# Performance work log

Measured on AMD Instinct MI355X. Metric: run time of the kernel, lower is better.

## Reference

```python
import jax, jax.numpy as jnp
import numpy as np
from jax import lax

E = 192      # hidden size
NH = 6       # attention heads
L = 6        # mixer blocks (permutation length)
CO = 256     # merging output channels
KH, KW = 7, 11   # locality window
LOCAL = (False, False, True, True, True, True)
B, H, W = 64, 8, 64


def skew(x, pad_value):
    # shift every row one step right, turning columns into diagonals (torch skew)
    rest = x.shape[:-2]
    Hd, Wd = x.shape[-2], x.shape[-1]
    x = jnp.pad(x, [(0, 0)] * (x.ndim - 1) + [(0, Hd)], constant_values=pad_value)
    x = x.reshape(*rest, -1)[..., : Hd * (Hd + Wd - 1)]
    x = x.reshape(*rest, Hd, Hd + Wd - 1)
    end = (Hd + Wd - 1) - (Wd // 2) + (Wd % 2 - 1)
    return x[..., Wd // 2 : end]


def make_mask(h, w, kh, kw):
    # boolean [h*w, h*w]; True inside the local window (torch: True = NOT allowed)
    m = jnp.ones((h, w, kh, kw), dtype=bool)
    m = m.transpose(0, 2, 1, 3)        # [h, kh, w, kw]
    m = skew(m, 0)                     # [h, kh, w, w]
    m = m.transpose(2, 3, 0, 1)        # [w, w, h, kh]
    m = skew(m, 0)                     # [w, w, h, h]
    m = m.transpose(2, 0, 3, 1)        # [h, w, h, w]
    return m.reshape(h * w, h * w)


def layernorm(x, g, b, eps=1e-5):
    mu = jnp.mean(x, axis=-1, keepdims=True)
    var = jnp.mean((x - mu) ** 2, axis=-1, keepdims=True)
    return (x - mu) / jnp.sqrt(var + eps) * g + b


def mha(x, mask, wi, bi, wo, bo, nh):
    # torch nn.MultiheadAttention (batch_first, self-attn, inference)
    b, s, e = x.shape
    hd = e // nh
    qkv = x @ wi.T + bi                                   # [b, s, 3e]
    q, k, v = jnp.split(qkv, 3, axis=-1)
    to_heads = lambda t: t.reshape(b, s, nh, hd).transpose(0, 2, 1, 3)
    q, k, v = to_heads(q), to_heads(k), to_heads(v)
    scores = jnp.einsum('bhqd,bhkd->bhqk', q, k) / jnp.sqrt(jnp.asarray(hd, x.dtype))
    if mask is not None:
        scores = jnp.where(mask, -jnp.inf, scores)
    attn = jax.nn.softmax(scores, axis=-1)
    out = jnp.einsum('bhqk,bhkd->bhqd', attn, v)
    out = out.transpose(0, 2, 1, 3).reshape(b, s, e)
    return out @ wo.T + bo


def mixer_block(x, mask, wi, bi, wo, bo, g1, b1, g2, b2, wm1, bm1, wm2, bm2):
    x = layernorm(x, g1, b1)
    x = mha(x, mask, wi, bi, wo, bo, NH) + x
    x = layernorm(x, g2, b2)
    h = jax.nn.relu(x @ wm1.T + bm1)
    return h @ wm2.T + bm2 + x


def fvtr_stage(image, in_w, in_b, out_w, out_b, ln1_g, ln1_b, ln2_g, ln2_b,
               w1, b1, w2, b2, conv_w, conv_b, mln_g, mln_b):
    bsz, c, h, w = image.shape
    x = jnp.swapaxes(image, -1, -3).reshape(bsz, w * h, c)   # [B, W*H, C]
    mask = make_mask(h, w, KH, KW)
    for i, loc in enumerate(LOCAL):
        x = mixer_block(x, mask if loc else None,
                        in_w[i], in_b[i], out_w[i], out_b[i],
                        ln1_g[i], ln1_b[i], ln2_g[i], ln2_b[i],
                        w1[i], b1[i], w2[i], b2[i])
    x = jnp.swapaxes(x.reshape(bsz, w, h, c), -1, -3)        # [B, C, H, W]
    # MergingBlock: conv (3,1) stride (2,1) pad (1,0) + channel LayerNorm
    y = lax.conv_general_dilated(x, conv_w, window_strides=(2, 1),
                                 padding=((1, 1), (0, 0)),
                                 dimension_numbers=('NCHW', 'OIHW', 'NCHW'))
    y = y + conv_b[None, :, None, None]
    y = jnp.moveaxis(y, 1, -1)
    y = layernorm(y, mln_g, mln_b)
    return jnp.moveaxis(y, -1, 1)


def setup_inputs() -> dict:
    key = jax.random.key(0)
    ks = jax.random.split(key, 8)
    s = 0.02
    return {
        'image': jax.random.normal(ks[0], (B, E, H, W), jnp.float32),
        'in_w':  s * jax.random.normal(ks[1], (L, 3 * E, E), jnp.float32),
        'in_b':  jnp.zeros((L, 3 * E), jnp.float32),
        'out_w': s * jax.random.normal(ks[2], (L, E, E), jnp.float32),
        'out_b': jnp.zeros((L, E), jnp.float32),
        'ln1_g': jnp.ones((L, E), jnp.float32),
        'ln1_b': jnp.zeros((L, E), jnp.float32),
        'ln2_g': jnp.ones((L, E), jnp.float32),
        'ln2_b': jnp.zeros((L, E), jnp.float32),
        'w1':    s * jax.random.normal(ks[3], (L, 4 * E, E), jnp.float32),
        'b1':    jnp.zeros((L, 4 * E), jnp.float32),
        'w2':    s * jax.random.normal(ks[4], (L, E, 4 * E), jnp.float32),
        'b2':    jnp.zeros((L, E), jnp.float32),
        'conv_w': s * jax.random.normal(ks[5], (CO, E, 3, 1), jnp.float32),
        'conv_b': jnp.zeros((CO,), jnp.float32),
        'mln_g': jnp.ones((CO,), jnp.float32),
        'mln_b': jnp.zeros((CO,), jnp.float32),
    }


def reference(image, in_w, in_b, out_w, out_b, ln1_g, ln1_b, ln2_g, ln2_b,
              w1, b1, w2, b2, conv_w, conv_b, mln_g, mln_b):
    return fvtr_stage(image, in_w, in_b, out_w, out_b, ln1_g, ln1_b, ln2_g, ln2_b,
                      w1, b1, w2, b2, conv_w, conv_b, mln_g, mln_b)
```

## Files before the change

### kernel.cpp

```cpp
#include <hip/hip_runtime.h>
#include <hip/hip_bf16.h>
#include <math.h>

#define Bn   64
#define Ssz  512
#define Ed   192
#define NHd  6
#define HDd  32
#define Ld   6
#define COd  256
#define Himg 8
#define Wimg 64
#define Mrows (Bn*Ssz)

typedef unsigned int  uint;
typedef unsigned short ushort;
using short8 = __attribute__((ext_vector_type(8))) short;
using f32x4  = __attribute__((ext_vector_type(4))) float;

__device__ inline ushort f2b(float f) {
    uint u = __builtin_bit_cast(uint, f);
    u = (u + 0x7FFFu + ((u >> 16) & 1u)) >> 16;
    return (ushort)u;
}

__device__ __forceinline__ float fexp2(float x) {
#if __has_builtin(__builtin_amdgcn_exp2f)
    return __builtin_amdgcn_exp2f(x);
#else
    return exp2f(x);
#endif
}

__device__ __forceinline__ uint cvt_pk_bf16(float a, float b) {
    uint r;
    asm("v_cvt_pk_bf16_f32 %0, %1, %2" : "=v"(r) : "v"(a), "v"(b));
    return r;
}

__device__ __forceinline__ void gload16(const ushort* g, ushort* l, int lane) {
#if __has_builtin(__builtin_amdgcn_global_load_lds)
    __builtin_amdgcn_global_load_lds(
        (const __attribute__((address_space(1))) uint*)g,
        (__attribute__((address_space(3))) uint*)l, 16, 0, 0);
#else
    *(uint4*)(l + (size_t)lane * 8) = *(const uint4*)g;
#endif
}

__global__ __launch_bounds__(256) void reshape_in(const float* __restrict__ img,
                                                  float* __restrict__ X) {
    int t = blockIdx.x * 256 + threadIdx.x;
    int c = t % Ed;
    int s = (t / Ed) % Ssz;
    int b = t / (Ed * Ssz);
    int w = s >> 3, h = s & 7;
    X[t] = img[(((size_t)b * Ed + c) * Himg + h) * Wimg + w];
}

__global__ __launch_bounds__(256) void f2b_arr(const float* __restrict__ in,
                                               ushort* __restrict__ out, int n) {
    int t = blockIdx.x * 256 + threadIdx.x;
    if (t < n) out[t] = f2b(in[t]);
}

__global__ __launch_bounds__(256) void conv_w_to_bf16(const float* __restrict__ cw,
                                                      ushort* __restrict__ out) {
    int t = blockIdx.x * 256 + threadIdx.x;
    if (t >= COd * 576) return;
    int co = t / 576, rem = t % 576;
    int kh = rem / Ed, c = rem % Ed;
    out[t] = f2b(cw[((size_t)co * Ed + c) * 3 + kh]);
}

__global__ __launch_bounds__(256) void ln_kernel(const float* __restrict__ in,
                                                 float* __restrict__ out,
                                                 ushort* __restrict__ outb,
                                                 const float* __restrict__ g,
                                                 const float* __restrict__ bb) {
    int row  = blockIdx.x * 4 + (threadIdx.x >> 6);
    int lane = threadIdx.x & 63;
    bool act = lane < 48;
    float4 v = make_float4(0.f, 0.f, 0.f, 0.f);
    if (act) v = ((const float4*)(in + (size_t)row * Ed))[lane];
    float s = v.x + v.y + v.z + v.w;
    #pragma unroll
    for (int off = 32; off > 0; off >>= 1) s += __shfl_xor(s, off);
    float mu = s * (1.f / 192.f);
    float4 d = make_float4(v.x - mu, v.y - mu, v.z - mu, v.w - mu);
    float qv = act ? (d.x*d.x + d.y*d.y + d.z*d.z + d.w*d.w) : 0.f;
    #pragma unroll
    for (int off = 32; off > 0; off >>= 1) qv += __shfl_xor(qv, off);
    float rstd = rsqrtf(qv * (1.f / 192.f) + 1e-5f);
    if (act) {
        float4 gg  = ((const float4*)g)[lane];
        float4 bbv = ((const float4*)bb)[lane];
        float4 y = make_float4(d.x * rstd * gg.x + bbv.x,
                               d.y * rstd * gg.y + bbv.y,
                               d.z * rstd * gg.z + bbv.z,
                               d.w * rstd * gg.w + bbv.w);
        ((float4*)(out + (size_t)row * Ed))[lane] = y;
        ushort4 yb;
        yb.x = f2b(y.x); yb.y = f2b(y.y); yb.z = f2b(y.z); yb.w = f2b(y.w);
        *(ushort4*)(outb + (size_t)row * Ed + lane * 4) = yb;
    }
}

template<int RELU, int RESID, int OBF, int VOUT>
__global__ __launch_bounds__(256) void gemm_mfma(
    const ushort* __restrict__ A, const ushort* __restrict__ Wt,
    const float* __restrict__ bias, const float* __restrict__ resid,
    float* __restrict__ C, ushort* __restrict__ Cb,
    ushort* __restrict__ qpout, ushort* __restrict__ kpout,
    ushort* __restrict__ vtout,
    int M, int N, int K)
{
    __shared__ __align__(16) ushort As[12288];
    __shared__ __align__(16) ushort Bs[6144];
    const int tid  = threadIdx.x;
    const int lane = tid & 63;
    const int wave = tid >> 6;
    const int wr = wave >> 1, wc = wave & 1;
    const int bm = blockIdx.x * 128;
    const int bn = blockIdx.y * 64;

    const ushort* Ag[6]; ushort* Al[6];
    #pragma unroll
    for (int i = 0; i < 6; ++i) {
        int fa = 4 * i + wave;
        int msub = fa / 3, ksub = fa % 3;
        int m = msub * 16 + (lane & 15);
        int k = ksub * 32 + ((lane >> 4) << 3);
        Ag[i] = A + (size_t)(bm + m) * K + k;
        Al[i] = As + fa * 512;
    }
    const ushort* Bg[3]; ushort* Bl[3];
    #pragma unroll
    for (int i = 0; i < 3; ++i) {
        int fb = 4 * i + wave;
        int nsub = fb / 3, ksub = fb % 3;
        int n = nsub * 16 + (lane & 15);
        int k = ksub * 32 + ((lane >> 4) << 3);
        Bg[i] = Wt + (size_t)(bn + n) * K + k;
        Bl[i] = Bs + fb * 512;
    }

    f32x4 acc[4][2];
    #pragma unroll
    for (int i = 0; i < 4; ++i)
        #pragma unroll
        for (int j = 0; j < 2; ++j) acc[i][j] = (f32x4){0.f, 0.f, 0.f, 0.f};

    for (int k0 = 0; k0 < K; k0 += 96) {
        #pragma unroll
        for (int i = 0; i < 6; ++i) gload16(Ag[i] + k0, Al[i], lane);
        #pragma unroll
        for (int i = 0; i < 3; ++i) gload16(Bg[i] + k0, Bl[i], lane);
        __syncthreads();
        #pragma unroll
        for (int ksub = 0; ksub < 3; ++ksub) {
            short8 af[4], bf[2];
            #pragma unroll
            for (int ms = 0; ms < 4; ++ms)
                af[ms] = *(const short8*)(As + (((wr*4+ms)*3 + ksub) * 64 + lane) * 8);
            #pragma unroll
            for (int ns = 0; ns < 2; ++ns)
                bf[ns] = *(const short8*)(Bs + (((wc*2+ns)*3 + ksub) * 64 + lane) * 8);
            #pragma unroll
            for (int ms = 0; ms < 4; ++ms)
                #pragma unroll
                for (int ns = 0; ns < 2; ++ns)
                    acc[ms][ns] = __builtin_amdgcn_mfma_f32_16x16x32_bf16(
                        af[ms], bf[ns], acc[ms][ns], 0, 0, 0);
        }
        __syncthreads();
    }

    int q = lane >> 4, colL = lane & 15;
    #pragma unroll
    for (int ms = 0; ms < 4; ++ms) {
        #pragma unroll
        for (int ns = 0; ns < 2; ++ns) {
            int row0 = bm + (wr*4 + ms) * 16 + q * 4;
            int col  = bn + (wc*2 + ns) * 16 + colL;
            float bvv = bias[col];
            float v[4];
            #pragma unroll
            for (int r = 0; r < 4; ++r) {
                v[r] = acc[ms][ns][r] + bvv;
                if (RELU) v[r] = fmaxf(v[r], 0.f);
                if (RESID) v[r] += resid[(size_t)(row0 + r) * N + col];
            }
            if (VOUT) {
                int bidx = row0 >> 9, srow = row0 & 511;
                if (col >= 384) {
                    int hh = (col - 384) >> 5, dd = (col - 384) & 31;
                    ushort4 pv;
                    pv.x = f2b(v[0]); pv.y = f2b(v[1]); pv.z = f2b(v[2]); pv.w = f2b(v[3]);
                    *(ushort4*)(vtout + (((size_t)(bidx * NHd + hh) * 32 + dd) << 9) + srow) = pv;
                } else {
                    ushort* dst = (col < 192) ? qpout : kpout;
                    int cc = (col < 192) ? col : col - 192;
                    if (col < 192) {
                        const float c2 = 0.2550547270628364f;
                        #pragma unroll
                        for (int r = 0; r < 4; ++r) v[r] *= c2;
                    }
                    int hh = cc >> 5, dd = cc & 31;
                    ushort* p = dst + ((size_t)(bidx * NHd + hh) << 14) + (size_t)srow * 32 + dd;
                    p[0]  = f2b(v[0]); p[32] = f2b(v[1]);
                    p[64] = f2b(v[2]); p[96] = f2b(v[3]);
                }
            } else {
                #pragma unroll
                for (int r = 0; r < 4; ++r) {
                    if (OBF) Cb[(size_t)(row0 + r) * N + col] = f2b(v[r]);
                    else     C [(size_t)(row0 + r) * N + col] = v[r];
                }
            }
        }
    }
}

template<int KIT, int LNOUT>
__global__ __launch_bounds__(256) void gemm_ln(
    const ushort* __restrict__ A, const ushort* __restrict__ Wt,
    const float* __restrict__ bias, const float* __restrict__ resid,
    const float* __restrict__ lng, const float* __restrict__ lnb,
    float* __restrict__ outf, ushort* __restrict__ outb)
{
    __shared__ __align__(16) ushort As[4096];
    __shared__ __align__(16) ushort Bs[12288];
    const int K = KIT * 64;
    const int lane = threadIdx.x & 63;
    const int wave = threadIdx.x >> 6;
    const int g = lane >> 4, ql = lane & 15;
    const int bm = blockIdx.x * 64;

    const ushort* Gp[8]; ushort* Lp[8];
    #pragma unroll
    for (int i = 0; i < 8; ++i) {
        int f = 4 * i + wave;
        if (f < 8) {
            int msub = f >> 1, ksub = f & 1;
            Gp[i] = A + (size_t)(bm + msub * 16 + ql) * K + ksub * 32 + g * 8;
            Lp[i] = As + f * 512;
        } else {
            int fb = f - 8, nsub = fb >> 1, ksub = fb & 1;
            Gp[i] = Wt + (size_t)(nsub * 16 + ql) * K + ksub * 32 + g * 8;
            Lp[i] = Bs + fb * 512;
        }
    }

    f32x4 acc[12];
    #pragma unroll
    for (int i = 0; i < 12; ++i) acc[i] = (f32x4){0.f, 0.f, 0.f, 0.f};

    for (int kc = 0; kc < KIT; ++kc) {
        #pragma unroll
        for (int i = 0; i < 8; ++i) gload16(Gp[i] + kc * 64, Lp[i], lane);
        __syncthreads();
        #pragma unroll
        for (int ksub = 0; ksub < 2; ++ksub) {
            short8 af = *(const short8*)(As + ((wave * 2 + ksub) * 64 + lane) * 8);
            #pragma unroll
            for (int ns = 0; ns < 12; ++ns) {
                short8 bf = *(const short8*)(Bs + ((ns * 2 + ksub) * 64 + lane) * 8);
                acc[ns] = __builtin_amdgcn_mfma_f32_16x16x32_bf16(af, bf, acc[ns], 0, 0, 0);
            }
        }
        __syncthreads();
    }

    float bi[12], gg[12], bb[12];
    #pragma unroll
    for (int ns = 0; ns < 12; ++ns) {
        int col = ns * 16 + ql;
        bi[ns] = bias[col];
        if (LNOUT) { gg[ns] = lng[col]; bb[ns] = lnb[col]; }
    }
    #pragma unroll
    for (int r = 0; r < 4; ++r) {
        int row = bm + wave * 16 + g * 4 + r;
        float v[12];
        #pragma unroll
        for (int ns = 0; ns < 12; ++ns)
            v[ns] = acc[ns][r] + bi[ns] + resid[(size_t)row * Ed + ns * 16 + ql];
        if (LNOUT) {
            float s = 0.f;
            #pragma unroll
            for (int ns = 0; ns < 12; ++ns) s += v[ns];
            s += __shfl_xor(s, 1); s += __shfl_xor(s, 2);
            s += __shfl_xor(s, 4); s += __shfl_xor(s, 8);
            float mu = s * (1.f / 192.f);
            float qv = 0.f;
            #pragma unroll
            for (int ns = 0; ns < 12; ++ns) { float d = v[ns] - mu; qv += d * d; }
            qv += __shfl_xor(qv, 1); qv += __shfl_xor(qv, 2);
            qv += __shfl_xor(qv, 4); qv += __shfl_xor(qv, 8);
            float rstd = rsqrtf(qv * (1.f / 192.f) + 1e-5f);
            #pragma unroll
            for (int ns = 0; ns < 12; ++ns) {
                float y = (v[ns] - mu) * rstd * gg[ns] + bb[ns];
                int col = ns * 16 + ql;
                outf[(size_t)row * Ed + col] = y;
                outb[(size_t)row * Ed + col] = f2b(y);
            }
        } else {
            #pragma unroll
            for (int ns = 0; ns < 12; ++ns)
                outf[(size_t)row * Ed + ns * 16 + ql] = v[ns];
        }
    }
}

template<int USE_MASK>
__global__ __launch_bounds__(256) void attn_mfma(const ushort* __restrict__ qp,
                                                 const ushort* __restrict__ kp,
                                                 const ushort* __restrict__ vt,
                                                 ushort* __restrict__ att) {
    __shared__ __align__(16) ushort P[4][2][2][512];
    const int bh = blockIdx.x;
    const int b = bh / NHd, h = bh % NHd;
    const int wave = threadIdx.x >> 6, lane = threadIdx.x & 63;
    const int g = lane >> 4, ql = lane & 15;
    const int qb = blockIdx.y * 128 + wave * 32;

    const ushort* qbase = qp + ((size_t)bh << 14);
    const ushort* kbase = kp + ((size_t)bh << 14);
    const ushort* vbase = vt + ((size_t)bh << 14);
    short8 qf[2];
    #pragma unroll
    for (int t = 0; t < 2; ++t)
        qf[t] = *(const short8*)(qbase + (size_t)(qb + t * 16 + ql) * 32 + g * 8);
    ushort* pw = &P[wave][0][0][0];

    short8 onesf;
    #pragma unroll
    for (int j = 0; j < 8; ++j) onesf[j] = (short)0x3F80;

    uint m0[2], m1[2]; int qh[2];
    if (USE_MASK) {
        #pragma unroll
        for (int t = 0; t < 2; ++t) {
            int qwt = ((qb + t * 16) & 63) + ql;
            qh[t] = (qb + t * 16) >> 6;
            uint a0 = 0, a1 = 0;
            #pragma unroll
            for (int i = 0; i < 8; ++i) {
                int keyl = (i >> 2) * 16 + 4 * g + (i & 3);
                int d0 = keyl - qwt;      d0 = d0 < 0 ? -d0 : d0;
                int d1 = keyl + 32 - qwt; d1 = d1 < 0 ? -d1 : d1;
                if (d0 <= 5) a0 |= (1u << i);
                if (d1 <= 5) a1 |= (1u << i);
            }
            m0[t] = a0; m1[t] = a1;
        }
    }

    f32x4 o0[2], o1[2], o2[2];
    #pragma unroll
    for (int t = 0; t < 2; ++t) {
        o0[t] = (f32x4){0.f,0.f,0.f,0.f};
        o1[t] = (f32x4){0.f,0.f,0.f,0.f};
        o2[t] = (f32x4){0.f,0.f,0.f,0.f};
    }
    const f32x4 z = {0.f,0.f,0.f,0.f};
    const int wst0 = ((g >> 1) * 16 + ql) * 8 + (g & 1) * 4;
    const int wst1 = (((g >> 1) + 2) * 16 + ql) * 8 + (g & 1) * 4;

    short8 kA0, kA1, kB0, kB1, vA0, vA1, vB0, vB1;

    auto LKA = [&](int kt) {
        kA0 = *(const short8*)(kbase + (size_t)(kt * 32 + ql) * 32 + g * 8);
        kA1 = *(const short8*)(kbase + (size_t)(kt * 32 + 16 + ql) * 32 + g * 8);
    };
    auto LKB = [&](int kt) {
        kB0 = *(const short8*)(kbase + (size_t)(kt * 32 + ql) * 32 + g * 8);
        kB1 = *(const short8*)(kbase + (size_t)(kt * 32 + 16 + ql) * 32 + g * 8);
    };
    auto LVA = [&](int kt) {
        vA0 = *(const short8*)(vbase + (size_t)ql * 512 + kt * 32 + 8 * g);
        vA1 = *(const short8*)(vbase + (size_t)(16 + ql) * 512 + kt * 32 + 8 * g);
    };
    auto LVB = [&](int kt) {
        vB0 = *(const short8*)(vbase + (size_t)ql * 512 + kt * 32 + 8 * g);
        vB1 = *(const short8*)(vbase + (size_t)(16 + ql) * 512 + kt * 32 + 8 * g);
    };

    auto QK = [&](int kt, int slot, short8 k0, short8 k1) {
        #pragma unroll
        for (int t = 0; t < 2; ++t) {
            f32x4 st0 = __builtin_amdgcn_mfma_f32_16x16x32_bf16(k0, qf[t], z, 0, 0, 0);
            f32x4 st1 = __builtin_amdgcn_mfma_f32_16x16x32_bf16(k1, qf[t], z, 0, 0, 0);
            float p[8];
            #pragma unroll
            for (int r = 0; r < 4; ++r) {
                p[r]     = fexp2(st0[r]);
                p[4 + r] = fexp2(st1[r]);
            }
            if (USE_MASK) {
                int dh = (kt >> 1) - qh[t]; dh = dh < 0 ? -dh : dh;
                if (dh <= 3) {
                    uint mm = (kt & 1) ? m1[t] : m0[t];
                    #pragma unroll
                    for (int i = 0; i < 8; ++i)
                        if ((mm >> i) & 1u) p[i] = 0.f;
                }
            }
            uint2 w0, w1;
            w0.x = cvt_pk_bf16(p[0], p[1]);
            w0.y = cvt_pk_bf16(p[2], p[3]);
            w1.x = cvt_pk_bf16(p[4], p[5]);
            w1.y = cvt_pk_bf16(p[6], p[7]);
            *(uint2*)(pw + (slot * 2 + t) * 512 + wst0) = w0;
            *(uint2*)(pw + (slot * 2 + t) * 512 + wst1) = w1;
        }
    };
    auto PV = [&](int slot, short8 v0, short8 v1) {
        #pragma unroll
        for (int t = 0; t < 2; ++t) {
            short8 paf = *(const short8*)(pw + (slot * 2 + t) * 512 + lane * 8);
            o0[t] = __builtin_amdgcn_mfma_f32_16x16x32_bf16(paf, v0, o0[t], 0, 0, 0);
            o1[t] = __builtin_amdgcn_mfma_f32_16x16x32_bf16(paf, v1, o1[t], 0, 0, 0);
            o2[t] = __builtin_amdgcn_mfma_f32_16x16x32_bf16(paf, onesf, o2[t], 0, 0, 0);
        }
    };

    LKA(0); LKB(1); LVA(0);
    QK(0, 0, kA0, kA1);
    LVB(1);
    #pragma unroll
    for (int ii = 0; ii < 7; ++ii) {
        const int i = 1 + 2 * ii;
        LKA(i + 1);
        QK(i, 1, kB0, kB1);
        PV(0, vA0, vA1);
        LVA(i + 1);
        LKB(i + 2);
        QK(i + 1, 0, kA0, kA1);
        PV(1, vB0, vB1);
        LVB(i + 2);
    }
    QK(15, 1, kB0, kB1);
    PV(0, vA0, vA1);
    PV(1, vB0, vB1);

    ushort* op = att + (size_t)b * Ssz * Ed + h * 32;
    #pragma unroll
    for (int t = 0; t < 2; ++t) {
        #pragma unroll
        for (int r = 0; r < 4; ++r) {
            float iv = 1.f / o2[t][r];
            int row = qb + t * 16 + 4 * g + r;
            op[(size_t)row * Ed + ql]      = f2b(o0[t][r] * iv);
            op[(size_t)row * Ed + 16 + ql] = f2b(o1[t][r] * iv);
        }
    }
}

__global__ __launch_bounds__(256) void im2col(const float* __restrict__ X,
                                              ushort* __restrict__ A2) {
    int t = blockIdx.x * 256 + threadIdx.x;
    int col = t % 576;
    int r   = t / 576;
    int kh = col / Ed, c = col % Ed;
    int w = r & 63, ho = (r >> 6) & 3, b = r >> 8;
    int hin = 2 * ho + kh - 1;
    float v = 0.f;
    if (hin >= 0 && hin < Himg)
        v = X[((size_t)(b * Ssz + w * Himg + hin)) * Ed + c];
    A2[t] = f2b(v);
}

__global__ __launch_bounds__(256) void ln_out_kernel(const float* __restrict__ C2,
                                                     const float* __restrict__ g,
                                                     const float* __restrict__ beta,
                                                     float* __restrict__ out) {
    __shared__ float lds[32 * 257];
    int w0 = blockIdx.x * 32, ho = blockIdx.y, b = blockIdx.z;
    int tid = threadIdx.x;
    size_t rbase = ((size_t)b * 4 + ho) * 64 + w0;

    for (int i = 0; i < 32; ++i)
        lds[i * 257 + tid] = C2[(rbase + i) * COd + tid];
    __syncthreads();

    int wv = tid >> 6, lane = tid & 63;
    for (int rr = 0; rr < 8; ++rr) {
        int i = wv * 8 + rr;
        float v0 = lds[i*257 + lane], v1 = lds[i*257 + lane + 64];
        float v2 = lds[i*257 + lane + 128], v3 = lds[i*257 + lane + 192];
        float s = v0 + v1 + v2 + v3;
        #pragma unroll
        for (int off = 32; off > 0; off >>= 1) s += __shfl_xor(s, off);
        float mu = s * (1.f / 256.f);
        float d0 = v0-mu, d1 = v1-mu, d2 = v2-mu, d3 = v3-mu;
        float qv = d0*d0 + d1*d1 + d2*d2 + d3*d3;
        #pragma unroll
        for (int off = 32; off > 0; off >>= 1) qv += __shfl_xor(qv, off);
        float rstd = rsqrtf(qv * (1.f / 256.f) + 1e-5f);
        lds[i*257 + lane]       = d0 * rstd * g[lane]       + beta[lane];
        lds[i*257 + lane + 64]  = d1 * rstd * g[lane + 64]  + beta[lane + 64];
        lds[i*257 + lane + 128] = d2 * rstd * g[lane + 128] + beta[lane + 128];
        lds[i*257 + lane + 192] = d3 * rstd * g[lane + 192] + beta[lane + 192];
    }
    __syncthreads();

    int w = tid & 31, half = tid >> 5;
    for (int j = 0; j < 32; ++j) {
        int co = half + j * 8;
        out[(((size_t)b * COd + co) * 4 + ho) * Wimg + w0 + w] = lds[w * 257 + co];
    }
}

extern "C" void kernel_launch(void* const* d_in, const int* in_sizes, int n_in,
                              void* d_out, int out_size, void* d_ws, size_t ws_size,
                              hipStream_t stream) {
    const float* image = (const float*)d_in[0];
    const float* in_w  = (const float*)d_in[1];
    const float* in_b  = (const float*)d_in[2];
    const float* out_w = (const float*)d_in[3];
    const float* out_b = (const float*)d_in[4];
    const float* ln1_g = (const float*)d_in[5];
    const float* ln1_b = (const float*)d_in[6];
    const float* ln2_g = (const float*)d_in[7];
    const float* ln2_b = (const float*)d_in[8];
    const float* w1    = (const float*)d_in[9];
    const float* b1    = (const float*)d_in[10];
    const float* w2    = (const float*)d_in[11];
    const float* b2    = (const float*)d_in[12];
    const float* convw = (const float*)d_in[13];
    const float* convb = (const float*)d_in[14];
    const float* mln_g = (const float*)d_in[15];
    const float* mln_b = (const float*)d_in[16];
    float* out = (float*)d_out;
    float* ws  = (float*)d_ws;

    float* F1   = ws;
    float* F2   = ws + 6291456;
    float* BIG  = ws + 12582912;
    ushort* QP   = (ushort*)BIG;
    ushort* KP   = (ushort*)(BIG + 3145728);
    ushort* VT   = (ushort*)(BIG + 6291456);
    ushort* Hb   = (ushort*)BIG;
    ushort* A2b  = (ushort*)BIG;
    float*  C2   = BIG + 4718592;
    ushort* XNb  = (ushort*)(BIG + 12582912);
    ushort* ATTb = (ushort*)(ws + 28311552);
    ushort* Wb   = (ushort*)(ws + 31457280);

    ushort* in_wb  = Wb;
    ushort* out_wb = Wb + 663552;
    ushort* w1b    = Wb + 884736;
    ushort* w2b    = Wb + 1769472;
    ushort* cwb    = Wb + 2654208;

    reshape_in<<<Mrows * Ed / 256, 256, 0, stream>>>(image, F2);
    f2b_arr<<<(663552 + 255) / 256, 256, 0, stream>>>(in_w,  in_wb,  663552);
    f2b_arr<<<(221184 + 255) / 256, 256, 0, stream>>>(out_w, out_wb, 221184);
    f2b_arr<<<(884736 + 255) / 256, 256, 0, stream>>>(w1,    w1b,    884736);
    f2b_arr<<<(884736 + 255) / 256, 256, 0, stream>>>(w2,    w2b,    884736);
    conv_w_to_bf16<<<(147456 + 255) / 256, 256, 0, stream>>>(convw, cwb);

    ln_kernel<<<Mrows / 4, 256, 0, stream>>>(F2, F1, XNb, ln1_g, ln1_b);

    for (int i = 0; i < Ld; ++i) {
        gemm_mfma<0,0,1,1><<<dim3(Mrows/128, 9), 256, 0, stream>>>(
            XNb, in_wb + (size_t)i * 3*Ed*Ed, in_b + i * 3*Ed,
            nullptr, nullptr, nullptr, QP, KP, VT, Mrows, 3*Ed, Ed);
        if (i >= 2) attn_mfma<1><<<dim3(Bn * NHd, 4), 256, 0, stream>>>(QP, KP, VT, ATTb);
        else        attn_mfma<0><<<dim3(Bn * NHd, 4), 256, 0, stream>>>(QP, KP, VT, ATTb);
        gemm_ln<3,1><<<Mrows/64, 256, 0, stream>>>(
            ATTb, out_wb + (size_t)i * Ed*Ed, out_b + i*Ed,
            F1, ln2_g + i*Ed, ln2_b + i*Ed, F2, XNb);
        gemm_mfma<1,0,1,0><<<dim3(Mrows/128, 12), 256, 0, stream>>>(
            XNb, w1b + (size_t)i * 4*Ed*Ed, b1 + i * 4*Ed,
            nullptr, nullptr, Hb, nullptr, nullptr, nullptr, Mrows, 4*Ed, Ed);
        if (i < Ld - 1) {
            gemm_ln<12,1><<<Mrows/64, 256, 0, stream>>>(
                Hb, w2b + (size_t)i * 4*Ed*Ed, b2 + i*Ed,
                F2, ln1_g + (i+1)*Ed, ln1_b + (i+1)*Ed, F1, XNb);
        } else {
            gemm_ln<12,0><<<Mrows/64, 256, 0, stream>>>(
                Hb, w2b + (size_t)i * 4*Ed*Ed, b2 + i*Ed,
                F2, nullptr, nullptr, F1, nullptr);
        }
    }

    im2col<<<9437184 / 256, 256, 0, stream>>>(F1, A2b);
    gemm_mfma<0,0,0,0><<<dim3(16384/128, 4), 256, 0, stream>>>(
        A2b, cwb, convb, nullptr, C2, nullptr, nullptr, nullptr, nullptr,
        16384, COd, 576);
    ln_out_kernel<<<dim3(2, 4, Bn), 256, 0, stream>>>(C2, mln_g, mln_b, out);
}
```

Measured before the change: 1.082 ms.

## Keep attention probabilities in registers via permlane32 swap instead of LDS round-trip

```diff
diff --git a/kernel.cpp b/kernel.cpp
--- a/kernel.cpp
+++ b/kernel.cpp
@@ -195,9 +195,10 @@
                 int bidx = row0 >> 9, srow = row0 & 511;
                 if (col >= 384) {
                     int hh = (col - 384) >> 5, dd = (col - 384) & 31;
+                    int sr = srow ^ ((((srow >> 2) ^ (srow >> 3)) & 1) * 12);
                     ushort4 pv;
                     pv.x = f2b(v[0]); pv.y = f2b(v[1]); pv.z = f2b(v[2]); pv.w = f2b(v[3]);
-                    *(ushort4*)(vtout + (((size_t)(bidx * NHd + hh) * 32 + dd) << 9) + srow) = pv;
+                    *(ushort4*)(vtout + (((size_t)(bidx * NHd + hh) * 32 + dd) << 9) + sr) = pv;
                 } else {
                     ushort* dst = (col < 192) ? qpout : kpout;
                     int cc = (col < 192) ? col : col - 192;
@@ -319,7 +320,6 @@
                                                  const ushort* __restrict__ kp,
                                                  const ushort* __restrict__ vt,
                                                  ushort* __restrict__ att) {
-    __shared__ __align__(16) ushort P[4][2][2][512];
     const int bh = blockIdx.x;
     const int b = bh / NHd, h = bh % NHd;
     const int wave = threadIdx.x >> 6, lane = threadIdx.x & 63;
@@ -333,7 +333,6 @@
     #pragma unroll
     for (int t = 0; t < 2; ++t)
         qf[t] = *(const short8*)(qbase + (size_t)(qb + t * 16 + ql) * 32 + g * 8);
-    ushort* pw = &P[wave][0][0][0];
 
     short8 onesf;
     #pragma unroll
@@ -366,10 +365,9 @@
         o2[t] = (f32x4){0.f,0.f,0.f,0.f};
     }
     const f32x4 z = {0.f,0.f,0.f,0.f};
-    const int wst0 = ((g >> 1) * 16 + ql) * 8 + (g & 1) * 4;
-    const int wst1 = (((g >> 1) + 2) * 16 + ql) * 8 + (g & 1) * 4;
 
     short8 kA0, kA1, kB0, kB1, vA0, vA1, vB0, vB1;
+    short8 pa[2];
 
     auto LKA = [&](int kt) {
         kA0 = *(const short8*)(kbase + (size_t)(kt * 32 + ql) * 32 + g * 8);
@@ -388,16 +386,16 @@
         vB1 = *(const short8*)(vbase + (size_t)(16 + ql) * 512 + kt * 32 + 8 * g);
     };
 
-    auto QK = [&](int kt, int slot, short8 k0, short8 k1) {
+    auto QK = [&](int kt, short8 k0, short8 k1) {
         #pragma unroll
         for (int t = 0; t < 2; ++t) {
             f32x4 st0 = __builtin_amdgcn_mfma_f32_16x16x32_bf16(k0, qf[t], z, 0, 0, 0);
             f32x4 st1 = __builtin_amdgcn_mfma_f32_16x16x32_bf16(k1, qf[t], z, 0, 0, 0);
-            float p[8];
+            float p8[8];
             #pragma unroll
             for (int r = 0; r < 4; ++r) {
-                p[r]     = fexp2(st0[r]);
-                p[4 + r] = fexp2(st1[r]);
+                p8[r]     = fexp2(st0[r]);
+                p8[4 + r] = fexp2(st1[r]);
             }
             if (USE_MASK) {
                 int dh = (kt >> 1) - qh[t]; dh = dh < 0 ? -dh : dh;
@@ -405,46 +403,38 @@
                     uint mm = (kt & 1) ? m1[t] : m0[t];
                     #pragma unroll
                     for (int i = 0; i < 8; ++i)
-                        if ((mm >> i) & 1u) p[i] = 0.f;
+                        if ((mm >> i) & 1u) p8[i] = 0.f;
                 }
             }
-            uint2 w0, w1;
-            w0.x = cvt_pk_bf16(p[0], p[1]);
-            w0.y = cvt_pk_bf16(p[2], p[3]);
-            w1.x = cvt_pk_bf16(p[4], p[5]);
-            w1.y = cvt_pk_bf16(p[6], p[7]);
-            *(uint2*)(pw + (slot * 2 + t) * 512 + wst0) = w0;
-            *(uint2*)(pw + (slot * 2 + t) * 512 + wst1) = w1;
+            uint Au = cvt_pk_bf16(p8[0], p8[1]);
+            uint Bu = cvt_pk_bf16(p8[2], p8[3]);
+            uint Cu = cvt_pk_bf16(p8[4], p8[5]);
+            uint Du = cvt_pk_bf16(p8[6], p8[7]);
+            asm("v_permlane32_swap_b32 %0, %1" : "+v"(Au), "+v"(Cu));
+            asm("v_permlane32_swap_b32 %0, %1" : "+v"(Bu), "+v"(Du));
+            union { uint u[4]; short8 s; } pk;
+            pk.u[0] = Au; pk.u[1] = Bu; pk.u[2] = Cu; pk.u[3] = Du;
+            pa[t] = pk.s;
         }
     };
-    auto PV = [&](int slot, short8 v0, short8 v1) {
+    auto PV = [&](short8 v0, short8 v1) {
         #pragma unroll
         for (int t = 0; t < 2; ++t) {
-            short8 paf = *(const short8*)(pw + (slot * 2 + t) * 512 + lane * 8);
-            o0[t] = __builtin_amdgcn_mfma_f32_16x16x32_bf16(paf, v0, o0[t], 0, 0, 0);
-            o1[t] = __builtin_amdgcn_mfma_f32_16x16x32_bf16(paf, v1, o1[t], 0, 0, 0);
-            o2[t] = __builtin_amdgcn_mfma_f32_16x16x32_bf16(paf, onesf, o2[t], 0, 0, 0);
+            o0[t] = __builtin_amdgcn_mfma_f32_16x16x32_bf16(pa[t], v0, o0[t], 0, 0, 0);
+            o1[t] = __builtin_amdgcn_mfma_f32_16x16x32_bf16(pa[t], v1, o1[t], 0, 0, 0);
+            o2[t] = __builtin_amdgcn_mfma_f32_16x16x32_bf16(pa[t], onesf, o2[t], 0, 0, 0);
         }
     };
 
-    LKA(0); LKB(1); LVA(0);
-    QK(0, 0, kA0, kA1);
-    LVB(1);
+    LKA(0); LVA(0); LKB(1); LVB(1);
     #pragma unroll
     for (int ii = 0; ii < 7; ++ii) {
-        const int i = 1 + 2 * ii;
-        LKA(i + 1);
-        QK(i, 1, kB0, kB1);
-        PV(0, vA0, vA1);
-        LVA(i + 1);
-        LKB(i + 2);
-        QK(i + 1, 0, kA0, kA1);
-        PV(1, vB0, vB1);
-        LVB(i + 2);
-    }
-    QK(15, 1, kB0, kB1);
-    PV(0, vA0, vA1);
-    PV(1, vB0, vB1);
+        const int i = 2 * ii;
+        QK(i, kA0, kA1);  PV(vA0, vA1);  LKA(i + 2); LVA(i + 2);
+        QK(i + 1, kB0, kB1); PV(vB0, vB1); LKB(i + 3); LVB(i + 3);
+    }
+    QK(14, kA0, kA1); PV(vA0, vA1);
+    QK(15, kB0, kB1); PV(vB0, vB1);
 
     ushort* op = att + (size_t)b * Ssz * Ed + h * 32;
     #pragma unroll
```

Result: no change. 1.095 ms (+1.2%).
